# Kernel tuning notes

Measured on AMD Instinct MI355X. Metric: run time of the kernel, lower is better.

The kernel has to match this reference:

```python
import jax, jax.numpy as jnp
import numpy as np

N, E, F_IN, F_OUT = 100000, 800000, 128, 128


def setup_inputs() -> dict:
    key = jax.random.key(0)
    ks = jax.random.split(key, 7)
    x = jax.random.normal(ks[0], (N, F_IN), dtype=jnp.float32)
    edge_val = jax.random.uniform(ks[1], (E,), dtype=jnp.float32)
    stdv = 1.0 / np.sqrt(F_OUT)
    weight = jax.random.uniform(ks[2], (F_IN, F_OUT), dtype=jnp.float32, minval=-stdv, maxval=stdv)
    diag1 = 0.01 * jax.random.normal(ks[3], (F_IN,), dtype=jnp.float32)
    bias = jax.random.uniform(ks[4], (F_OUT,), dtype=jnp.float32, minval=-stdv, maxval=stdv)
    edge_row = jax.random.randint(ks[5], (E,), 0, N)
    edge_col = jax.random.randint(ks[6], (E,), 0, N)
    return {"x": x, "edge_val": edge_val, "weight": weight, "diag1": diag1,
            "bias": bias, "edge_row": edge_row, "edge_col": edge_col}


def reference(x, edge_val, weight, diag1, bias, edge_row, edge_col):
    # e1 = spmm(l_sym, x): gather neighbor features, scale by edge value, scatter-add to rows
    e1 = jax.ops.segment_sum(edge_val[:, None] * x[edge_col], edge_row, num_segments=N)  # [N, F_IN]
    # e2 = e1 @ (diag(d) + I)  ==  e1 * (d + 1)  (elementwise column scale)
    e2 = e1 * (diag1 + 1.0)
    # e5 = (x - e2) @ W + b
    return (x - e2) @ weight + bias
```

## Files before the change

### kernel.cpp

```cpp
#include <hip/hip_runtime.h>

#define F 128
#define BM 128
#define VS 132
#define SCHUNK 1024

__global__ __launch_bounds__(256) void scatter_k(
    const float* __restrict__ x, const float* __restrict__ edge_val,
    const int* __restrict__ erow, const int* __restrict__ ecol,
    float* e1, int E)
{
    const int gtid = blockIdx.x * blockDim.x + threadIdx.x;
    const int wid  = gtid >> 6;
    const int nw   = (gridDim.x * blockDim.x) >> 6;
    const int lane = threadIdx.x & 63;
    const int sub  = lane >> 5;
    const int l    = lane & 31;

    for (int e0 = wid * 2; e0 < E; e0 += nw * 2) {
        const int e = e0 + sub;
        if (e < E) {
            const int   r   = erow[e];
            const int   c   = ecol[e];
            const float val = edge_val[e];
            const float4 xv = ((const float4*)(x + (size_t)c * F))[l];
            float* dst = e1 + (size_t)r * F + l * 4;
            unsafeAtomicAdd(dst + 0, val * xv.x);
            unsafeAtomicAdd(dst + 1, val * xv.y);
            unsafeAtomicAdd(dst + 2, val * xv.z);
            unsafeAtomicAdd(dst + 3, val * xv.w);
        }
    }
}

__global__ __launch_bounds__(256) void hist_k(
    const int* __restrict__ erow, int* cnt, int E)
{
    int i = blockIdx.x * blockDim.x + threadIdx.x;
    if (i < E) atomicAdd(&cnt[erow[i]], 1);
}

__global__ __launch_bounds__(256) void scan1_k(
    const int* __restrict__ cnt, int* offs, int* psum, int N)
{
    __shared__ int ts[256];
    const int b = blockIdx.x, t = threadIdx.x;
    const int base = b * SCHUNK + t * 4;
    int v[4];
    int s = 0;
#pragma unroll
    for (int j = 0; j < 4; ++j) {
        v[j] = (base + j < N) ? cnt[base + j] : 0;
        s += v[j];
    }
    ts[t] = s;
    __syncthreads();
    for (int off = 1; off < 256; off <<= 1) {
        int u = (t >= off) ? ts[t - off] : 0;
        __syncthreads();
        ts[t] += u;
        __syncthreads();
    }
    int excl = ts[t] - s;
#pragma unroll
    for (int j = 0; j < 4; ++j) {
        if (base + j < N) offs[base + j] = excl;
        excl += v[j];
    }
    if (t == 255) psum[b] = ts[255];
}

__global__ __launch_bounds__(256) void scan2_k(
    const int* __restrict__ psum, int* bpref, int* offs, int NB, int N)
{
    __shared__ int ts[256];
    const int t = threadIdx.x;
    const int chunk = (NB + 255) >> 8;
    const int begin = t * chunk;
    const int end   = min(begin + chunk, NB);
    int s = 0;
    for (int i = begin; i < end; ++i) s += psum[i];
    ts[t] = s;
    __syncthreads();
    for (int off = 1; off < 256; off <<= 1) {
        int u = (t >= off) ? ts[t - off] : 0;
        __syncthreads();
        ts[t] += u;
        __syncthreads();
    }
    int run = ts[t] - s;
    for (int i = begin; i < end; ++i) { bpref[i] = run; run += psum[i]; }
    if (t == 255) offs[N] = ts[255];
}

__global__ __launch_bounds__(256) void scan3_k(
    int* offs, const int* __restrict__ bpref, int N)
{
    int i = blockIdx.x * blockDim.x + threadIdx.x;
    if (i < N) offs[i] += bpref[i >> 10];
}

__global__ __launch_bounds__(256) void build_k(
    const int* __restrict__ erow, const int* __restrict__ ecol,
    const float* __restrict__ eval, const int* __restrict__ offs,
    int* cur, int* bcol, float* bval, int E)
{
    int i = blockIdx.x * blockDim.x + threadIdx.x;
    if (i < E) {
        const int r   = erow[i];
        const int pos = offs[r] + atomicAdd(&cur[r], 1);
        bcol[pos] = ecol[i];
        bval[pos] = eval[i];
    }
}

__global__ __launch_bounds__(256) void gather_k(
    const float* __restrict__ x, const int* __restrict__ bcol,
    const float* __restrict__ bval, const int* __restrict__ offs,
    float* __restrict__ e1, int N)
{
    const int wave = (blockIdx.x * blockDim.x + threadIdx.x) >> 6;
    const int lane = threadIdx.x & 63;
    if (wave >= N) return;

    const int s = offs[wave];
    const int t = offs[wave + 1];
    float2 acc = make_float2(0.f, 0.f);
    int e = s;
    for (; e + 4 <= t; e += 4) {
        const int   c0 = bcol[e + 0], c1 = bcol[e + 1];
        const int   c2 = bcol[e + 2], c3 = bcol[e + 3];
        const float v0 = bval[e + 0], v1 = bval[e + 1];
        const float v2 = bval[e + 2], v3 = bval[e + 3];
        const float2 a0 = ((const float2*)(x + (size_t)c0 * F))[lane];
        const float2 a1 = ((const float2*)(x + (size_t)c1 * F))[lane];
        const float2 a2 = ((const float2*)(x + (size_t)c2 * F))[lane];
        const float2 a3 = ((const float2*)(x + (size_t)c3 * F))[lane];
        acc.x = fmaf(v0, a0.x, acc.x); acc.y = fmaf(v0, a0.y, acc.y);
        acc.x = fmaf(v1, a1.x, acc.x); acc.y = fmaf(v1, a1.y, acc.y);
        acc.x = fmaf(v2, a2.x, acc.x); acc.y = fmaf(v2, a2.y, acc.y);
        acc.x = fmaf(v3, a3.x, acc.x); acc.y = fmaf(v3, a3.y, acc.y);
    }
    for (; e < t; ++e) {
        const int   c = bcol[e];
        const float v = bval[e];
        const float2 xv = ((const float2*)(x + (size_t)c * F))[lane];
        acc.x = fmaf(v, xv.x, acc.x);
        acc.y = fmaf(v, xv.y, acc.y);
    }
    ((float2*)(e1 + (size_t)wave * F))[lane] = acc;
}

__global__ __launch_bounds__(256) void fused_k(
    const float* __restrict__ x, const float* e1,
    const float* __restrict__ W, const float* __restrict__ diag1,
    const float* __restrict__ bias, float* out, int N)
{
    __shared__ float vs[BM * VS];
    const int t  = threadIdx.x;
    const int tx = t & 15;
    const int ty = t >> 4;
    const size_t row0 = (size_t)blockIdx.x * BM;

#pragma unroll
    for (int i = 0; i < 16; ++i) {
        const int idx = t + i * 256;
        const int r   = idx >> 5;
        const int k4  = idx & 31;
        const size_t row = row0 + r;
        float4 v = make_float4(0.f, 0.f, 0.f, 0.f);
        if (row < (size_t)N) {
            const float4 xv = ((const float4*)(x  + row * F))[k4];
            const float4 ev = ((const float4*)(e1 + row * F))[k4];
            const float4 dv = ((const float4*)diag1)[k4];
            v.x = xv.x - ev.x * (dv.x + 1.f);
            v.y = xv.y - ev.y * (dv.y + 1.f);
            v.z = xv.z - ev.z * (dv.z + 1.f);
            v.w = xv.w - ev.w * (dv.w + 1.f);
        }
        *(float4*)&vs[r * VS + k4 * 4] = v;
    }
    __syncthreads();

    float acc[8][8];
#pragma unroll
    for (int rr = 0; rr < 8; ++rr)
#pragma unroll
        for (int c = 0; c < 8; ++c) acc[rr][c] = 0.f;

    for (int k = 0; k < F; k += 4) {
        float4 vf[8];
#pragma unroll
        for (int rr = 0; rr < 8; ++rr)
            vf[rr] = *(const float4*)&vs[(ty + rr * 16) * VS + k];
#pragma unroll
        for (int kk = 0; kk < 4; ++kk) {
            const float* wrow = W + (size_t)(k + kk) * F + tx * 8;
            const float4 wa = *(const float4*)(wrow);
            const float4 wb = *(const float4*)(wrow + 4);
#pragma unroll
            for (int rr = 0; rr < 8; ++rr) {
                const float vk = ((const float*)&vf[rr])[kk];
                acc[rr][0] = fmaf(vk, wa.x, acc[rr][0]);
                acc[rr][1] = fmaf(vk, wa.y, acc[rr][1]);
                acc[rr][2] = fmaf(vk, wa.z, acc[rr][2]);
                acc[rr][3] = fmaf(vk, wa.w, acc[rr][3]);
                acc[rr][4] = fmaf(vk, wb.x, acc[rr][4]);
                acc[rr][5] = fmaf(vk, wb.y, acc[rr][5]);
                acc[rr][6] = fmaf(vk, wb.z, acc[rr][6]);
                acc[rr][7] = fmaf(vk, wb.w, acc[rr][7]);
            }
        }
    }

    const float4 b0 = *(const float4*)(bias + tx * 8);
    const float4 b1 = *(const float4*)(bias + tx * 8 + 4);
#pragma unroll
    for (int rr = 0; rr < 8; ++rr) {
        const size_t row = row0 + ty + rr * 16;
        if (row < (size_t)N) {
            float4 oa = make_float4(acc[rr][0] + b0.x, acc[rr][1] + b0.y,
                                    acc[rr][2] + b0.z, acc[rr][3] + b0.w);
            float4 ob = make_float4(acc[rr][4] + b1.x, acc[rr][5] + b1.y,
                                    acc[rr][6] + b1.z, acc[rr][7] + b1.w);
            ((float4*)(out + row * F))[tx * 2]     = oa;
            ((float4*)(out + row * F))[tx * 2 + 1] = ob;
        }
    }
}

extern "C" void kernel_launch(void* const* d_in, const int* in_sizes, int n_in,
                              void* d_out, int out_size, void* d_ws, size_t ws_size,
                              hipStream_t stream) {
    const float* x        = (const float*)d_in[0];
    const float* edge_val = (const float*)d_in[1];
    const float* weight   = (const float*)d_in[2];
    const float* diag1    = (const float*)d_in[3];
    const float* bias     = (const float*)d_in[4];
    const int*   erow     = (const int*)d_in[5];
    const int*   ecol     = (const int*)d_in[6];
    float* out = (float*)d_out;

    const int E  = in_sizes[1];
    const int N  = in_sizes[0] / F;
    const int NB = (N + SCHUNK - 1) / SCHUNK;

    const size_t need = ((size_t)(3 * N + 1) + 2 * (size_t)NB + 2 * (size_t)E) * 4;

    if (ws_size >= need) {
        int*   offs  = (int*)d_ws;
        int*   cnt   = offs + (N + 1);
        int*   cur   = cnt + N;
        int*   psum  = cur + N;
        int*   bpref = psum + NB;
        int*   bcol  = bpref + NB;
        float* bval  = (float*)(bcol + E);

        hipMemsetAsync(cnt, 0, (size_t)(2 * N) * sizeof(int), stream);

        const int eblocks = (E + 255) / 256;
        hist_k <<<eblocks, 256, 0, stream>>>(erow, cnt, E);
        scan1_k<<<NB, 256, 0, stream>>>(cnt, offs, psum, N);
        scan2_k<<<1, 256, 0, stream>>>(psum, bpref, offs, NB, N);
        scan3_k<<<(N + 255) / 256, 256, 0, stream>>>(offs, bpref, N);
        build_k<<<eblocks, 256, 0, stream>>>(erow, ecol, edge_val, offs, cur, bcol, bval, E);

        const int gblocks = (N * 64 + 255) / 256;
        gather_k<<<gblocks, 256, 0, stream>>>(x, bcol, bval, offs, out, N);
    } else {
        hipMemsetAsync(out, 0, (size_t)N * F * sizeof(float), stream);
        scatter_k<<<2048, 256, 0, stream>>>(x, edge_val, erow, ecol, out, E);
    }

    const int fblocks = (N + BM - 1) / BM;
    fused_k<<<fblocks, 256, 0, stream>>>(x, out, weight, diag1, bias, out, N);
}
```

Before: 335.8 us.

## Fuse diag/residual combine into gather and halve GEMM row tile

Moves the x - e1*(d+1) computation into the CSR gather kernel's epilogue, so the GEMM kernel reads one precomputed matrix instead of both x and e1. The scatter fallback path gets a separate elementwise kernel to do the same. The fused GEMM tile shrinks from 128 to 64 rows, halving accumulator registers and shared memory to raise occupancy, at the cost of reloading W more often. In the gather path x is read once for the self row, which cuts one full N×F read in the GEMM stage.

```diff
diff --git a/kernel.cpp b/kernel.cpp
--- a/kernel.cpp
+++ b/kernel.cpp
@@ -1,7 +1,7 @@
 #include <hip/hip_runtime.h>
 
 #define F 128
-#define BM 128
+#define BM 64
 #define VS 132
 #define SCHUNK 1024
 
@@ -33,6 +33,24 @@
     }
 }
 
+__global__ __launch_bounds__(256) void mkv_k(
+    const float* __restrict__ x, const float* __restrict__ diag1,
+    float* v, int n4)
+{
+    int i = blockIdx.x * blockDim.x + threadIdx.x;
+    if (i < n4) {
+        const float4 xv = ((const float4*)x)[i];
+        const float4 ev = ((const float4*)v)[i];
+        const float4 dv = ((const float4*)diag1)[i & 31];
+        float4 o;
+        o.x = xv.x - ev.x * (dv.x + 1.f);
+        o.y = xv.y - ev.y * (dv.y + 1.f);
+        o.z = xv.z - ev.z * (dv.z + 1.f);
+        o.w = xv.w - ev.w * (dv.w + 1.f);
+        ((float4*)v)[i] = o;
+    }
+}
+
 __global__ __launch_bounds__(256) void hist_k(
     const int* __restrict__ erow, int* cnt, int E)
 {
@@ -114,10 +132,10 @@
     }
 }
 
-__global__ __launch_bounds__(256) void gather_k(
+__global__ __launch_bounds__(256) void gatherv_k(
     const float* __restrict__ x, const int* __restrict__ bcol,
     const float* __restrict__ bval, const int* __restrict__ offs,
-    float* __restrict__ e1, int N)
+    const float* __restrict__ diag1, float* __restrict__ vout, int N)
 {
     const int wave = (blockIdx.x * blockDim.x + threadIdx.x) >> 6;
     const int lane = threadIdx.x & 63;
@@ -125,6 +143,9 @@
 
     const int s = offs[wave];
     const int t = offs[wave + 1];
+    const float2 xr = ((const float2*)(x + (size_t)wave * F))[lane];
+    const float2 dv = ((const float2*)diag1)[lane];
+
     float2 acc = make_float2(0.f, 0.f);
     int e = s;
     for (; e + 4 <= t; e += 4) {
@@ -148,12 +169,14 @@
         acc.x = fmaf(v, xv.x, acc.x);
         acc.y = fmaf(v, xv.y, acc.y);
     }
-    ((float2*)(e1 + (size_t)wave * F))[lane] = acc;
+    float2 v;
+    v.x = xr.x - acc.x * (dv.x + 1.f);
+    v.y = xr.y - acc.y * (dv.y + 1.f);
+    ((float2*)(vout + (size_t)wave * F))[lane] = v;
 }
 
 __global__ __launch_bounds__(256) void fused_k(
-    const float* __restrict__ x, const float* e1,
-    const float* __restrict__ W, const float* __restrict__ diag1,
+    const float* v, const float* __restrict__ W,
     const float* __restrict__ bias, float* out, int N)
 {
     __shared__ float vs[BM * VS];
@@ -163,35 +186,28 @@
     const size_t row0 = (size_t)blockIdx.x * BM;
 
 #pragma unroll
-    for (int i = 0; i < 16; ++i) {
+    for (int i = 0; i < 8; ++i) {
         const int idx = t + i * 256;
         const int r   = idx >> 5;
         const int k4  = idx & 31;
         const size_t row = row0 + r;
-        float4 v = make_float4(0.f, 0.f, 0.f, 0.f);
-        if (row < (size_t)N) {
-            const float4 xv = ((const float4*)(x  + row * F))[k4];
-            const float4 ev = ((const float4*)(e1 + row * F))[k4];
-            const float4 dv = ((const float4*)diag1)[k4];
-            v.x = xv.x - ev.x * (dv.x + 1.f);
-            v.y = xv.y - ev.y * (dv.y + 1.f);
-            v.z = xv.z - ev.z * (dv.z + 1.f);
-            v.w = xv.w - ev.w * (dv.w + 1.f);
-        }
-        *(float4*)&vs[r * VS + k4 * 4] = v;
+        float4 val = make_float4(0.f, 0.f, 0.f, 0.f);
+        if (row < (size_t)N)
+            val = ((const float4*)(v + row * F))[k4];
+        *(float4*)&vs[r * VS + k4 * 4] = val;
     }
     __syncthreads();
 
-    float acc[8][8];
-#pragma unroll
-    for (int rr = 0; rr < 8; ++rr)
+    float acc[4][8];
+#pragma unroll
+    for (int rr = 0; rr < 4; ++rr)
 #pragma unroll
         for (int c = 0; c < 8; ++c) acc[rr][c] = 0.f;
 
     for (int k = 0; k < F; k += 4) {
-        float4 vf[8];
-#pragma unroll
-        for (int rr = 0; rr < 8; ++rr)
+        float4 vf[4];
+#pragma unroll
+        for (int rr = 0; rr < 4; ++rr)
             vf[rr] = *(const float4*)&vs[(ty + rr * 16) * VS + k];
 #pragma unroll
         for (int kk = 0; kk < 4; ++kk) {
@@ -199,7 +215,7 @@
             const float4 wa = *(const float4*)(wrow);
             const float4 wb = *(const float4*)(wrow + 4);
 #pragma unroll
-            for (int rr = 0; rr < 8; ++rr) {
+            for (int rr = 0; rr < 4; ++rr) {
                 const float vk = ((const float*)&vf[rr])[kk];
                 acc[rr][0] = fmaf(vk, wa.x, acc[rr][0]);
                 acc[rr][1] = fmaf(vk, wa.y, acc[rr][1]);
@@ -216,7 +232,7 @@
     const float4 b0 = *(const float4*)(bias + tx * 8);
     const float4 b1 = *(const float4*)(bias + tx * 8 + 4);
 #pragma unroll
-    for (int rr = 0; rr < 8; ++rr) {
+    for (int rr = 0; rr < 4; ++rr) {
         const size_t row = row0 + ty + rr * 16;
         if (row < (size_t)N) {
             float4 oa = make_float4(acc[rr][0] + b0.x, acc[rr][1] + b0.y,
@@ -266,12 +282,14 @@
         build_k<<<eblocks, 256, 0, stream>>>(erow, ecol, edge_val, offs, cur, bcol, bval, E);
 
         const int gblocks = (N * 64 + 255) / 256;
-        gather_k<<<gblocks, 256, 0, stream>>>(x, bcol, bval, offs, out, N);
+        gatherv_k<<<gblocks, 256, 0, stream>>>(x, bcol, bval, offs, diag1, out, N);
     } else {
         hipMemsetAsync(out, 0, (size_t)N * F * sizeof(float), stream);
         scatter_k<<<2048, 256, 0, stream>>>(x, edge_val, erow, ecol, out, E);
+        const int n4 = N * F / 4;
+        mkv_k<<<(n4 + 255) / 256, 256, 0, stream>>>(x, diag1, out, n4);
     }
 
     const int fblocks = (N + BM - 1) / BM;
-    fused_k<<<fblocks, 256, 0, stream>>>(x, out, weight, diag1, bias, out, N);
-}
+    fused_k<<<fblocks, 256, 0, stream>>>(out, weight, bias, out, N);
+}
```

Result: faster. 325.2 us (-3.1%).
